# Kernel optimization log

Hardware: AMD Instinct MI355X
Metric: run time of the kernel (lower is better)

The kernel has to match this reference:

```python
import jax, jax.numpy as jnp
import numpy as np

K = 3
KK = K * K
EPS = 1e-5


def conv2d(x, w, b, pad):
    y = jax.lax.conv_general_dilated(x, w, (1, 1), [(pad, pad), (pad, pad)],
                                     dimension_numbers=("NCHW", "OIHW", "NCHW"))
    return y + b[None, :, None, None]


def bn(x, g, b, m, v):
    inv = g / jnp.sqrt(v + EPS)
    return x * inv[None, :, None, None] + (b - m * inv)[None, :, None, None]


def deform_sample(x, dy, dx):
    # x: [B,C,H,W]; dy,dx: [B,KK,H,W] -> sampled [B,C,KK,H,W] (bilinear, zeros outside)
    B, C, H, W = x.shape
    k = jnp.arange(K, dtype=x.dtype) - 1.0  # pad=1, dilation=1, stride=1
    ky = jnp.repeat(k, K)  # [KK] row offsets
    kx = jnp.tile(k, K)    # [KK] col offsets
    hh = jnp.arange(H, dtype=x.dtype)
    ww = jnp.arange(W, dtype=x.dtype)
    py = hh[None, :, None] + ky[:, None, None] + dy  # [B,KK,H,W]
    px = ww[None, None, :] + kx[:, None, None] + dx

    def sample_one(img, py, px):
        y0f = jnp.floor(py); x0f = jnp.floor(px)
        wy = py - y0f; wx = px - x0f
        y0 = y0f.astype(jnp.int32); x0 = x0f.astype(jnp.int32)

        def gather(yi, xi, w):
            valid = (yi >= 0) & (yi < H) & (xi >= 0) & (xi < W)
            yc = jnp.clip(yi, 0, H - 1); xc = jnp.clip(xi, 0, W - 1)
            v = img[:, yc, xc]  # [C,KK,H,W]
            return v * (w * valid)[None]

        return (gather(y0, x0, (1 - wy) * (1 - wx)) +
                gather(y0, x0 + 1, (1 - wy) * wx) +
                gather(y0 + 1, x0, wy * (1 - wx)) +
                gather(y0 + 1, x0 + 1, wy * wx))

    return jax.vmap(sample_one)(x, py, px)


def setup_inputs() -> dict:
    key = jax.random.key(0)
    ks = jax.random.split(key, 16)
    B, C, H, W = 8, 256, 64, 64
    d = {
        "feature": jax.random.normal(ks[0], (B, C, H, W), jnp.float32),
        "p1_w": jax.random.normal(ks[1], (C, C, 1, 1), jnp.float32) * 0.05,
        "p1_b": jax.random.normal(ks[2], (C,), jnp.float32) * 0.05,
        "bn1_g": jax.random.normal(ks[3], (C,), jnp.float32) * 0.1 + 1.0,
        "bn1_b": jax.random.normal(ks[4], (C,), jnp.float32) * 0.05,
        "bn1_m": jax.random.normal(ks[5], (C,), jnp.float32) * 0.05,
        "bn1_v": jax.random.uniform(ks[6], (C,), jnp.float32) + 0.5,
        "off_w": jax.random.normal(ks[7], (3 * KK, 2 * C, K, K), jnp.float32) * 0.01,
        "off_b": jax.random.normal(ks[8], (3 * KK,), jnp.float32) * 0.01,
        "dcn_w": jax.random.normal(ks[9], (C, C, K, K), jnp.float32) * 0.05,
        "dcn_b": jax.random.normal(ks[10], (C,), jnp.float32) * 0.05,
        "bn2_g": jax.random.normal(ks[11], (C,), jnp.float32) * 0.1 + 1.0,
        "bn2_b": jax.random.normal(ks[12], (C,), jnp.float32) * 0.05,
        "bn2_m": jax.random.normal(ks[13], (C,), jnp.float32) * 0.05,
        "bn2_v": jax.random.uniform(ks[14], (C,), jnp.float32) + 0.5,
    }
    return d


def reference(feature, p1_w, p1_b, bn1_g, bn1_b, bn1_m, bn1_v,
              off_w, off_b, dcn_w, dcn_b, bn2_g, bn2_b, bn2_m, bn2_v):
    flipped = feature[..., ::-1]                      # flip last (W) axis
    proj = bn(conv2d(feature, p1_w, p1_b, 0), bn1_g, bn1_b, bn1_m, bn1_v)
    # DCNv2: offsets/mask from concat(flipped, proj)
    concat = jnp.concatenate([flipped, proj], axis=1)
    off = conv2d(concat, off_w, off_b, 1)             # [B,27,H,W]
    dy = off[:, :KK]
    dx = off[:, KK:2 * KK]
    mask = jax.nn.sigmoid(off[:, 2 * KK:])            # [B,KK,H,W]
    sampled = deform_sample(flipped, dy, dx)          # [B,C,KK,H,W]
    O = dcn_w.shape[0]
    y = jnp.einsum("bckhw,ock->bohw", sampled * mask[:, None], dcn_w.reshape(O, -1, KK))
    y = y + dcn_b[None, :, None, None]
    y = bn(y, bn2_g, bn2_b, bn2_m, bn2_v)
    return jax.nn.relu(proj + y)
```

## Files before the change

kernel.cpp:

```cpp
#include <hip/hip_runtime.h>
#include <hip/hip_bf16.h>
#include <math.h>

typedef __attribute__((ext_vector_type(8))) short short8;
typedef __attribute__((ext_vector_type(4))) short short4v;
typedef __attribute__((ext_vector_type(4))) float f32x4;
typedef __attribute__((ext_vector_type(2))) float f32x2;

__device__ __forceinline__ float bs2f(short s){
    union { unsigned u; float f; } x; x.u = ((unsigned)(unsigned short)s) << 16; return x.f;
}
__device__ __forceinline__ short f2bs(float f){
    union { float f; unsigned u; } x; x.f = f;
    unsigned r = x.u + 0x7fff + ((x.u >> 16) & 1);
    return (short)(r >> 16);
}
__device__ __forceinline__ f32x2 up2(unsigned u){
    union { unsigned u; float f; } lo, hi;
    lo.u = u << 16; hi.u = u & 0xffff0000u;
    f32x2 r; r.x = lo.f; r.y = hi.f; return r;
}
__device__ __forceinline__ unsigned pk2rn(float lo, float hi){
    __hip_bfloat162 h = __float22bfloat162_rn(make_float2(lo, hi));
    union { __hip_bfloat162 h; unsigned u; } cv; cv.h = h; return cv.u;
}
__device__ __forceinline__ void gl2lds16(const void* g, void* l){
    __builtin_amdgcn_global_load_lds(
        (const __attribute__((address_space(1))) void*)g,
        (__attribute__((address_space(3))) void*)l, 16, 0, 0);
}
__device__ __forceinline__ void hard_barrier(){
    __builtin_amdgcn_sched_barrier(0);
    __builtin_amdgcn_s_barrier();
    __builtin_amdgcn_sched_barrier(0);
}

#define XPB ((size_t)66*66*512)


__global__ void k_prep(const float* __restrict__ p1_w, const float* __restrict__ p1_b,
                       const float* __restrict__ bn1_g, const float* __restrict__ bn1_b,
                       const float* __restrict__ bn1_m, const float* __restrict__ bn1_v,
                       const float* __restrict__ off_w,
                       const float* __restrict__ dcn_w, const float* __restrict__ dcn_b,
                       const float* __restrict__ bn2_g, const float* __restrict__ bn2_b,
                       const float* __restrict__ bn2_m, const float* __restrict__ bn2_v,
                       short* __restrict__ p1_wb, short* __restrict__ Woffb,
                       short* __restrict__ Wbf,
                       float* __restrict__ bias1f, float* __restrict__ inv2f,
                       float* __restrict__ bias2f, unsigned* __restrict__ XpadU)
{
    int blk = blockIdx.x, t = threadIdx.x;
    if (blk == 0) {
        float inv1 = bn1_g[t] / sqrtf(bn1_v[t] + 1e-5f);
        bias1f[t] = p1_b[t] * inv1 + bn1_b[t] - bn1_m[t] * inv1;
        float inv2 = bn2_g[t] / sqrtf(bn2_v[t] + 1e-5f);
        inv2f[t] = inv2;
        bias2f[t] = dcn_b[t] * inv2 + bn2_b[t] - bn2_m[t] * inv2;
    } else if (blk <= 256) {
        int ci = blk - 1;
        float inv1 = bn1_g[t] / sqrtf(bn1_v[t] + 1e-5f);
        p1_wb[t*256 + ci] = f2bs(p1_w[t*256 + ci] * inv1);
    } else if (blk <= 2560) {
        int ck = blk - 257;
        int c = ck / 9, tap = ck % 9;
        Wbf[t*2304 + tap*256 + c] = f2bs(dcn_w[t*2304 + ck]);
    } else if (blk <= 7168) {
        int e = blk - 2561;
        if (t < 32) {
            int tap = e >> 9, ci = e & 511;
            float v = off_w[((t < 27) ? t : 0)*4608 + ci*9 + tap];
            Woffb[t*4608 + e] = (t < 27) ? f2bs(v) : (short)0;
        }
    } else {
        int hb = blk - 7169;
        int b = hb / 260, i = hb % 260;
        int y, x;
        if (i < 66)       { y = 0;  x = i; }
        else if (i < 132) { y = 65; x = i - 66; }
        else { int j = i - 132; y = 1 + (j >> 1); x = (j & 1) * 65; }
        XpadU[((size_t)(b*66 + y)*66 + x)*256 + t] = 0u;
    }
}

__global__ void k_featT(const float* __restrict__ feature, short* __restrict__ Xpad)
{
    __shared__ float tile[64][65];
    int bb = blockIdx.x;
    int cg = bb & 3, h = (bb >> 2) & 63, b = bb >> 8;
    int c0 = cg * 64;
    int t = threadIdx.x;
    int lw = t & 63, li = t >> 6;
    #pragma unroll
    for (int j = 0; j < 16; ++j) {
        int cl = j*4 + li;
        tile[cl][63 - lw] = feature[((b*256 + c0 + cl)*64 + h)*64 + lw];
    }
    __syncthreads();
    #pragma unroll
    for (int j = 0; j < 16; ++j) {
        int wl = j*4 + li;
        Xpad[((size_t)(b*66 + h+1)*66 + (wl+1))*512 + c0 + lw] = f2bs(tile[lw][wl]);
    }
}

__global__ __launch_bounds__(512, 4) void k_projm(
    short* Xpad, const short* __restrict__ p1_wb, const float* __restrict__ bias1f)
{
    __shared__ short Ash[256*32];
    __shared__ short Bsh[64*32];
    int bid = blockIdx.x;
    int b = bid >> 6, h = bid & 63;
    int t = threadIdx.x;
    int lane = t & 63, w = t >> 6;
    int ln = lane & 15, q = lane >> 4;
    int r16 = lane >> 2;
    int sq  = (lane & 3) ^ ((lane >> 3) & 3);
    int rq  = (q ^ ((ln >> 1) & 3)) * 8;
    size_t rowbase = (size_t)(b*66 + h + 1)*66;

    f32x4 acc[2][4] = {};
    for (int kt = 0; kt < 8; ++kt) {
        int kcol = kt*32 + sq*8;
        #pragma unroll
        for (int i = 0; i < 2; ++i) {
            int row = w*32 + i*16 + r16;
            gl2lds16(p1_wb + (size_t)row*256 + kcol, Ash + (w*32 + i*16)*32);
        }
        if (w < 4) {
            int x = w*16 + r16;
            gl2lds16(Xpad + (rowbase + (64 - x))*512 + kcol, Bsh + (w*16)*32);
        }
        __syncthreads();
        short8 af[2], bfr[4];
        #pragma unroll
        for (int i = 0; i < 2; ++i)
            af[i] = *(const short8*)&Ash[(w*32 + i*16 + ln)*32 + rq];
        #pragma unroll
        for (int j = 0; j < 4; ++j)
            bfr[j] = *(const short8*)&Bsh[(j*16 + ln)*32 + rq];
        #pragma unroll
        for (int i = 0; i < 2; ++i)
            #pragma unroll
            for (int j = 0; j < 4; ++j)
                acc[i][j] = __builtin_amdgcn_mfma_f32_16x16x32_bf16(af[i], bfr[j], acc[i][j], 0, 0, 0);
        __syncthreads();
    }
    #pragma unroll
    for (int i = 0; i < 2; ++i) {
        int ob = w*32 + i*16 + q*4;
        #pragma unroll
        for (int j = 0; j < 4; ++j) {
            int x = j*16 + ln;
            size_t xb = (rowbase + x + 1)*512 + 256 + ob;
            short4v st;
            st.x = f2bs(acc[i][j][0] + bias1f[ob]);
            st.y = f2bs(acc[i][j][1] + bias1f[ob+1]);
            st.z = f2bs(acc[i][j][2] + bias1f[ob+2]);
            st.w = f2bs(acc[i][j][3] + bias1f[ob+3]);
            *(short4v*)&Xpad[xb] = st;
        }
    }
}

__global__ __launch_bounds__(512, 4) void k_offm(
    const short* __restrict__ Xpad, const short* __restrict__ Woffb,
    const float* __restrict__ off_b, float* __restrict__ offv)
{
    __shared__ short Ash[2][4][32*32];
    __shared__ short Bsh[2][4][64*32];
    int bid = blockIdx.x;
    int b = bid >> 6, h = bid & 63;
    int t = threadIdx.x;
    int lane = t & 63, w = t >> 6;
    int ln = lane & 15, q = lane >> 4;
    int wr = w >> 2, wc = w & 3;
    int r16 = lane >> 2;
    int sq  = (lane & 3) ^ ((lane >> 3) & 3);
    int rq  = (q ^ ((ln >> 1) & 3)) * 8;
    const short* xb = Xpad + (size_t)b*XPB;

    auto STAGE = [&](int it, int pb){
        int tap = it >> 2, c0 = (it & 3) << 7;
        int dy = tap/3 - 1, dx = tap%3 - 1;
        #pragma unroll
        for (int s = 0; s < 4; ++s) {
            int cc = c0 + s*32 + sq*8;
            if (w < 4) {
                int row = w*16 + r16;
                const short* gB = xb + ((size_t)(h + 1 + dy)*66 + (row + dx + 1))*512 + cc;
                gl2lds16(gB, &Bsh[pb][s][(w*16)*32]);
            } else if (w < 6) {
                int row = (w-4)*16 + r16;
                const short* gA = Woffb + (size_t)row*4608 + tap*512 + cc;
                gl2lds16(gA, &Ash[pb][s][((w-4)*16)*32]);
            }
        }
    };

    f32x4 acc = {};
    STAGE(0, 0);
    asm volatile("s_waitcnt vmcnt(0)" ::: "memory");
    hard_barrier();
    for (int it = 0; it < 36; ++it) {
        int pb = it & 1;
        if (it < 35) STAGE(it + 1, pb ^ 1);
        __builtin_amdgcn_sched_barrier(0);
        #pragma unroll
        for (int s = 0; s < 4; ++s) {
            short8 af  = *(const short8*)&Ash[pb][s][(wr*16 + ln)*32 + rq];
            short8 bfr = *(const short8*)&Bsh[pb][s][(wc*16 + ln)*32 + rq];
            acc = __builtin_amdgcn_mfma_f32_16x16x32_bf16(af, bfr, acc, 0, 0, 0);
        }
        asm volatile("s_waitcnt vmcnt(0) lgkmcnt(0)" ::: "memory");
        hard_barrier();
    }
    int x = wc*16 + ln;
    #pragma unroll
    for (int r = 0; r < 4; ++r) {
        int oc = wr*16 + q*4 + r;
        if (oc < 27)
            offv[((b*27 + oc)*64 + h)*64 + x] = acc[r] + off_b[oc];
    }
}

__global__ __launch_bounds__(512, 4) void k_gemm(
    const short* __restrict__ Xpad,
    const short* __restrict__ Wbf,
    const float* __restrict__ offv,
    const float* __restrict__ inv2f, const float* __restrict__ bias2f,
    float* __restrict__ out)
{
    __shared__ __align__(16) short Ash[2][256*32];
    __shared__ __align__(16) short Bsh[2][64*32];
    __shared__ unsigned c_pk[576];
    __shared__ float c_w[576*4];
    int bid = blockIdx.x;
    int b = bid & 7, h = bid >> 3;
    int t = threadIdx.x;
    int lane = t & 63, w = t >> 6;
    int ln = lane & 15, q = lane >> 4;
    int r16 = lane >> 2;
    int sq  = (lane & 3) ^ ((lane >> 3) & 3);
    int rq  = (q ^ ((ln >> 1) & 3)) * 8;

    for (int e = t; e < 576; e += 512) {
        int p = e / 9, k = e % 9;
        int base = (b*27)*4096 + h*64 + p;
        float dy = offv[base + k*4096];
        float dx = offv[base + (9+k)*4096];
        float ms = offv[base + (18+k)*4096];
        ms = 1.f / (1.f + expf(-ms));
        float py = (float)h + (float)(k/3 - 1) + dy;
        float px = (float)p + (float)(k%3 - 1) + dx;
        float y0f = floorf(py), x0f = floorf(px);
        float wy = py - y0f, wx = px - x0f;
        int y0 = (int)y0f, x0 = (int)x0f;
        int y1 = y0 + 1, x1 = x0 + 1;
        float vy0 = (y0 >= 0 && y0 < 64) ? 1.f : 0.f;
        float vy1 = (y1 >= 0 && y1 < 64) ? 1.f : 0.f;
        float vx0 = (x0 >= 0 && x0 < 64) ? 1.f : 0.f;
        float vx1 = (x1 >= 0 && x1 < 64) ? 1.f : 0.f;
        int y0c = min(max(y0,0),63), y1c = min(max(y1,0),63);
        int x0c = min(max(x0,0),63), x1c = min(max(x1,0),63);
        unsigned cell = (unsigned)(((y0c+1)*66 + x0c+1)*128);
        unsigned sx = (x1c != x0c) ? 1u : 0u;
        unsigned sy = (y1c != y0c) ? 1u : 0u;
        c_pk[e] = cell | (sx << 20) | (sy << 21);
        c_w[e*4+0] = ms * (1.f-wy)*(1.f-wx) * vy0*vx0;
        c_w[e*4+1] = ms * (1.f-wy)*wx       * vy0*vx1;
        c_w[e*4+2] = ms * wy*(1.f-wx)       * vy1*vx0;
        c_w[e*4+3] = ms * wy*wx             * vy1*vx1;
    }
    __syncthreads();

    const uint2* fT = (const uint2*)Xpad + (size_t)b*(XPB/4);
    int pr = t >> 3;
    int jo = t & 7;
    int pe9 = pr*9;
    short* bdst = &Bsh[jo >> 2][pr*32 + (((jo & 3) ^ ((pr >> 1) & 3)) << 3)];

    f32x4 acc[2][4] = {};
    uint4 U[4], V[4];

    auto GATHER = [&](int win, uint4 (&dst)[4]) {
        unsigned pw = c_pk[pe9 + (win >> 2)];
        int o00 = pw & 0xFFFFF;
        int dxs = (pw >> 13) & 128;
        int dys = ((pw >> 8) & 0x2000) | ((pw >> 13) & 0x100);
        int cin = ((win & 3) << 4) + jo*2;
        const uint2* p0 = fT + (o00 + cin);
        dst[0] = *(const uint4*)(p0);
        dst[1] = *(const uint4*)(p0 + dxs);
        dst[2] = *(const uint4*)(p0 + dys);
        dst[3] = *(const uint4*)(p0 + dys + dxs);
    };

    auto WIN = [&](int kc2, uint4 (&uc)[4], uint4 (&vn)[4]) {
        int tap = kc2 >> 2;
        #pragma unroll
        for (int s = 0; s < 2; ++s) {
            int kcol = (kc2*2 + s)*32 + sq*8;
            #pragma unroll
            for (int i = 0; i < 2; ++i) {
                int row = w*32 + i*16 + r16;
                gl2lds16(Wbf + (size_t)row*2304 + kcol, &Ash[s][(w*32 + i*16)*32]);
            }
        }
        __builtin_amdgcn_sched_barrier(0);
        GATHER(kc2 < 35 ? kc2 + 1 : 35, vn);
        const float4 cw = *(const float4*)&c_w[(pe9 + tap)*4];
        f32x2 Wx; Wx.x = cw.x; Wx.y = cw.x;
        f32x2 Wy; Wy.x = cw.y; Wy.y = cw.y;
        f32x2 Wz; Wz.x = cw.z; Wz.y = cw.z;
        f32x2 Ww; Ww.x = cw.w; Ww.y = cw.w;
        f32x2 G0 = Wx*up2(uc[0].x) + Wy*up2(uc[1].x) + Wz*up2(uc[2].x) + Ww*up2(uc[3].x);
        f32x2 G1 = Wx*up2(uc[0].y) + Wy*up2(uc[1].y) + Wz*up2(uc[2].y) + Ww*up2(uc[3].y);
        f32x2 G2 = Wx*up2(uc[0].z) + Wy*up2(uc[1].z) + Wz*up2(uc[2].z) + Ww*up2(uc[3].z);
        f32x2 G3 = Wx*up2(uc[0].w) + Wy*up2(uc[1].w) + Wz*up2(uc[2].w) + Ww*up2(uc[3].w);
        uint4 pkv;
        pkv.x = pk2rn(G0.x, G0.y);
        pkv.y = pk2rn(G1.x, G1.y);
        pkv.z = pk2rn(G2.x, G2.y);
        pkv.w = pk2rn(G3.x, G3.y);
        *(uint4*)bdst = pkv;
        asm volatile("s_waitcnt vmcnt(4) lgkmcnt(0)" ::: "memory");
        hard_barrier();
        #pragma unroll
        for (int s = 0; s < 2; ++s) {
            short8 af[2], bfr[4];
            #pragma unroll
            for (int i = 0; i < 2; ++i)
                af[i] = *(const short8*)&Ash[s][(w*32 + i*16 + ln)*32 + rq];
            #pragma unroll
            for (int jj = 0; jj < 4; ++jj)
                bfr[jj] = *(const short8*)&Bsh[s][(jj*16 + ln)*32 + rq];
            #pragma unroll
            for (int i = 0; i < 2; ++i)
                #pragma unroll
                for (int jj = 0; jj < 4; ++jj)
                    acc[i][jj] = __builtin_amdgcn_mfma_f32_16x16x32_bf16(af[i], bfr[jj], acc[i][jj], 0, 0, 0);
        }
        hard_barrier();
    };

    GATHER(0, U);
    __builtin_amdgcn_sched_barrier(0);
    for (int kc2 = 0; kc2 < 36; kc2 += 2) {
        WIN(kc2, U, V);
        WIN(kc2 + 1, V, U);
    }

    #pragma unroll
    for (int i = 0; i < 2; ++i) {
        int ob = w*32 + i*16 + q*4;
        #pragma unroll
        for (int jj = 0; jj < 4; ++jj) {
            int p = jj*16 + ln;
            size_t xb = ((size_t)(b*66 + h + 1)*66 + p + 1)*512 + 256 + ob;
            short4v prr = *(const short4v*)&Xpad[xb];
            #pragma unroll
            for (int r = 0; r < 4; ++r) {
                int o = ob + r;
                size_t idx = ((size_t)(b*256 + o))*4096 + h*64 + p;
                float rs = bs2f(((const short*)&prr)[r]);
                float v = rs + acc[i][jj][r]*inv2f[o] + bias2f[o];
                out[idx] = v < 0.f ? 0.f : v;
            }
        }
    }
}

extern "C" void kernel_launch(void* const* d_in, const int* in_sizes, int n_in,
                              void* d_out, int out_size, void* d_ws, size_t ws_size,
                              hipStream_t stream)
{
    const float* feature = (const float*)d_in[0];
    const float* p1_w  = (const float*)d_in[1];
    const float* p1_b  = (const float*)d_in[2];
    const float* bn1_g = (const float*)d_in[3];
    const float* bn1_b = (const float*)d_in[4];
    const float* bn1_m = (const float*)d_in[5];
    const float* bn1_v = (const float*)d_in[6];
    const float* off_w = (const float*)d_in[7];
    const float* off_b = (const float*)d_in[8];
    const float* dcn_w = (const float*)d_in[9];
    const float* dcn_b = (const float*)d_in[10];
    const float* bn2_g = (const float*)d_in[11];
    const float* bn2_b = (const float*)d_in[12];
    const float* bn2_m = (const float*)d_in[13];
    const float* bn2_v = (const float*)d_in[14];

    float* ws = (float*)d_ws;
    short* Xpad   = (short*)ws;
    float* offbuf = ws + 8921088;
    short* p1_wb  = (short*)(ws + 9805824);
    short* Woffb  = (short*)(ws + 9838592);
    short* Wbf    = (short*)(ws + 9912320);
    float* bias1f = ws + 10207232;
    float* inv2f  = ws + 10207488;
    float* bias2f = ws + 10207744;

    k_prep<<<9249, 256, 0, stream>>>(p1_w, p1_b, bn1_g, bn1_b, bn1_m, bn1_v,
                                     off_w, dcn_w, dcn_b, bn2_g, bn2_b, bn2_m, bn2_v,
                                     p1_wb, Woffb, Wbf, bias1f, inv2f, bias2f,
                                     (unsigned*)Xpad);
    k_featT<<<2048, 256, 0, stream>>>(feature, Xpad);
    k_projm<<<512, 512, 0, stream>>>(Xpad, p1_wb, bias1f);
    k_offm<<<512, 512, 0, stream>>>(Xpad, Woffb, off_b, offbuf);
    k_gemm<<<512, 512, 0, stream>>>(Xpad, Wbf, offbuf, inv2f, bias2f, (float*)d_out);
}
```

Measured before the change: 235.5 us.

## Restructure weight prep, reorder block-to-batch mapping, single-buffer offset conv

The weight-prep kernel now assigns one block per output row with threads spanning the contiguous dimension, which gives coalesced writes and cuts the grid from 9249 blocks to 2625. The transpose, projection and offset kernels change their block index mapping so consecutive blocks cover different batches at the same row. The offset convolution drops its double-buffered, manually synchronised pipeline in favour of single-buffered stages of 8 slices with __syncthreads, halving the iteration count. That last change gives up overlap of loads and MFMA work in exchange for fewer barriers and deeper per-stage batching.

```diff
diff --git a/kernel.cpp b/kernel.cpp
--- a/kernel.cpp
+++ b/kernel.cpp
@@ -58,22 +58,31 @@
         inv2f[t] = inv2;
         bias2f[t] = dcn_b[t] * inv2 + bn2_b[t] - bn2_m[t] * inv2;
     } else if (blk <= 256) {
-        int ci = blk - 1;
-        float inv1 = bn1_g[t] / sqrtf(bn1_v[t] + 1e-5f);
-        p1_wb[t*256 + ci] = f2bs(p1_w[t*256 + ci] * inv1);
-    } else if (blk <= 2560) {
-        int ck = blk - 257;
-        int c = ck / 9, tap = ck % 9;
-        Wbf[t*2304 + tap*256 + c] = f2bs(dcn_w[t*2304 + ck]);
-    } else if (blk <= 7168) {
-        int e = blk - 2561;
-        if (t < 32) {
-            int tap = e >> 9, ci = e & 511;
-            float v = off_w[((t < 27) ? t : 0)*4608 + ci*9 + tap];
-            Woffb[t*4608 + e] = (t < 27) ? f2bs(v) : (short)0;
+        int o = blk - 1;
+        float inv1 = bn1_g[o] / sqrtf(bn1_v[o] + 1e-5f);
+        p1_wb[o*256 + t] = f2bs(p1_w[o*256 + t] * inv1);
+    } else if (blk <= 512) {
+        int o = blk - 257;
+        const float* src = dcn_w + (size_t)o*2304;
+        #pragma unroll
+        for (int j = 0; j < 9; ++j)
+            Wbf[(size_t)o*2304 + j*256 + t] = f2bs(src[t*9 + j]);
+    } else if (blk <= 544) {
+        int oc = blk - 513;
+        if (oc < 27) {
+            const float* src = off_w + (size_t)oc*4608;
+            #pragma unroll
+            for (int j = 0; j < 18; ++j) {
+                int e = j*256 + t, tap = e >> 9, ci = e & 511;
+                Woffb[(size_t)oc*4608 + e] = f2bs(src[ci*9 + tap]);
+            }
+        } else {
+            #pragma unroll
+            for (int j = 0; j < 18; ++j)
+                Woffb[(size_t)oc*4608 + j*256 + t] = 0;
         }
     } else {
-        int hb = blk - 7169;
+        int hb = blk - 545;
         int b = hb / 260, i = hb % 260;
         int y, x;
         if (i < 66)       { y = 0;  x = i; }
@@ -87,7 +96,7 @@
 {
     __shared__ float tile[64][65];
     int bb = blockIdx.x;
-    int cg = bb & 3, h = (bb >> 2) & 63, b = bb >> 8;
+    int b = bb & 7, h = (bb >> 3) & 63, cg = bb >> 9;
     int c0 = cg * 64;
     int t = threadIdx.x;
     int lw = t & 63, li = t >> 6;
@@ -110,7 +119,7 @@
     __shared__ short Ash[256*32];
     __shared__ short Bsh[64*32];
     int bid = blockIdx.x;
-    int b = bid >> 6, h = bid & 63;
+    int b = bid & 7, h = bid >> 3;
     int t = threadIdx.x;
     int lane = t & 63, w = t >> 6;
     int ln = lane & 15, q = lane >> 4;
@@ -167,10 +176,10 @@
     const short* __restrict__ Xpad, const short* __restrict__ Woffb,
     const float* __restrict__ off_b, float* __restrict__ offv)
 {
-    __shared__ short Ash[2][4][32*32];
-    __shared__ short Bsh[2][4][64*32];
+    __shared__ short Ash[8][32*32];
+    __shared__ short Bsh[8][64*32];
     int bid = blockIdx.x;
-    int b = bid >> 6, h = bid & 63;
+    int b = bid & 7, h = bid >> 3;
     int t = threadIdx.x;
     int lane = t & 63, w = t >> 6;
     int ln = lane & 15, q = lane >> 4;
@@ -180,40 +189,32 @@
     int rq  = (q ^ ((ln >> 1) & 3)) * 8;
     const short* xb = Xpad + (size_t)b*XPB;
 
-    auto STAGE = [&](int it, int pb){
-        int tap = it >> 2, c0 = (it & 3) << 7;
-        int dy = tap/3 - 1, dx = tap%3 - 1;
-        #pragma unroll
-        for (int s = 0; s < 4; ++s) {
-            int cc = c0 + s*32 + sq*8;
+    f32x4 acc = {};
+    for (int it = 0; it < 18; ++it) {
+        #pragma unroll
+        for (int s = 0; s < 8; ++s) {
+            int k = it*256 + s*32;
+            int tap = k >> 9;
+            int dy = tap/3 - 1, dx = tap%3 - 1;
             if (w < 4) {
                 int row = w*16 + r16;
-                const short* gB = xb + ((size_t)(h + 1 + dy)*66 + (row + dx + 1))*512 + cc;
-                gl2lds16(gB, &Bsh[pb][s][(w*16)*32]);
+                const short* gB = xb + ((size_t)(h + 1 + dy)*66 + (row + dx + 1))*512
+                                     + (k & 511) + sq*8;
+                gl2lds16(gB, &Bsh[s][(w*16)*32]);
             } else if (w < 6) {
                 int row = (w-4)*16 + r16;
-                const short* gA = Woffb + (size_t)row*4608 + tap*512 + cc;
-                gl2lds16(gA, &Ash[pb][s][((w-4)*16)*32]);
+                const short* gA = Woffb + (size_t)row*4608 + k + sq*8;
+                gl2lds16(gA, &Ash[s][((w-4)*16)*32]);
             }
         }
-    };
-
-    f32x4 acc = {};
-    STAGE(0, 0);
-    asm volatile("s_waitcnt vmcnt(0)" ::: "memory");
-    hard_barrier();
-    for (int it = 0; it < 36; ++it) {
-        int pb = it & 1;
-        if (it < 35) STAGE(it + 1, pb ^ 1);
-        __builtin_amdgcn_sched_barrier(0);
-        #pragma unroll
-        for (int s = 0; s < 4; ++s) {
-            short8 af  = *(const short8*)&Ash[pb][s][(wr*16 + ln)*32 + rq];
-            short8 bfr = *(const short8*)&Bsh[pb][s][(wc*16 + ln)*32 + rq];
+        __syncthreads();
+        #pragma unroll
+        for (int s = 0; s < 8; ++s) {
+            short8 af  = *(const short8*)&Ash[s][(wr*16 + ln)*32 + rq];
+            short8 bfr = *(const short8*)&Bsh[s][(wc*16 + ln)*32 + rq];
             acc = __builtin_amdgcn_mfma_f32_16x16x32_bf16(af, bfr, acc, 0, 0, 0);
         }
-        asm volatile("s_waitcnt vmcnt(0) lgkmcnt(0)" ::: "memory");
-        hard_barrier();
+        __syncthreads();
     }
     int x = wc*16 + ln;
     #pragma unroll
@@ -401,7 +402,7 @@
     float* inv2f  = ws + 10207488;
     float* bias2f = ws + 10207744;
 
-    k_prep<<<9249, 256, 0, stream>>>(p1_w, p1_b, bn1_g, bn1_b, bn1_m, bn1_v,
+    k_prep<<<2625, 256, 0, stream>>>(p1_w, p1_b, bn1_g, bn1_b, bn1_m, bn1_v,
                                      off_w, dcn_w, dcn_b, bn2_g, bn2_b, bn2_m, bn2_v,
                                      p1_wb, Woffb, Wbf, bias1f, inv2f, bias2f,
                                      (unsigned*)Xpad);
```

New measurement: 218.9 us. -7.0%, faster.
